# Optimization experiments

Measured on AMD Instinct MI355X. Metric: run time of the kernel, lower is better.

The kernel has to match this reference:

```python
import jax, jax.numpy as jnp
import numpy as np

N = 50000        # nodes
E = 800000       # edges (avg degree 16)
OBS = 128        # observation_dim
HID = 64         # hidden_dim (per head)
H1 = 4           # heads in conv1
ACT = 32         # action_dim
NEG_SLOPE = 0.2  # GATv2 default negative_slope


def setup_inputs() -> dict:
    key = jax.random.key(0)
    ks = jax.random.split(key, 10)
    s = 0.05
    x = jax.random.normal(ks[0], (N, OBS), jnp.float32)
    edge_index = jax.random.randint(ks[1], (2, E), 0, N, dtype=jnp.int32)
    # conv1: GATv2Conv(OBS -> HID, heads=4, concat=True)
    W1l = jax.random.normal(ks[2], (OBS, H1 * HID), jnp.float32) * s  # lin_l (source)
    W1r = jax.random.normal(ks[3], (OBS, H1 * HID), jnp.float32) * s  # lin_r (target)
    att1 = jax.random.normal(ks[4], (H1, HID), jnp.float32) * s
    b1 = jnp.zeros((H1 * HID,), jnp.float32)
    # conv2: GATv2Conv(H1*HID -> ACT, heads=1, concat=False)
    W2l = jax.random.normal(ks[5], (H1 * HID, ACT), jnp.float32) * s
    W2r = jax.random.normal(ks[6], (H1 * HID, ACT), jnp.float32) * s
    att2 = jax.random.normal(ks[7], (1, ACT), jnp.float32) * s
    b2 = jnp.zeros((ACT,), jnp.float32)
    return {"x": x, "edge_index": edge_index, "W1l": W1l, "W1r": W1r,
            "att1": att1, "b1": b1, "W2l": W2l, "W2r": W2r,
            "att2": att2, "b2": b2}


def gatv2_layer(x, Wl, Wr, att, bias, src, dst, heads, out_ch, concat):
    """PyG GATv2Conv (add_self_loops=False, share_weights=False)."""
    n = x.shape[0]
    xl = (x @ Wl).reshape(n, heads, out_ch)  # source transform
    xr = (x @ Wr).reshape(n, heads, out_ch)  # target transform
    e = xl[src] + xr[dst]                    # [E, H, C] gathered messages
    g = jnp.where(e > 0, e, NEG_SLOPE * e)   # LeakyReLU
    logits = jnp.einsum('ehc,hc->eh', g, att)  # [E, H]
    # segment softmax over incoming edges of each destination node
    m = jax.ops.segment_max(logits, dst, num_segments=n)      # [N, H]
    ex = jnp.exp(logits - m[dst])
    denom = jax.ops.segment_sum(ex, dst, num_segments=n)      # [N, H]
    alpha = ex / denom[dst]                                   # [E, H]
    out = jax.ops.segment_sum(xl[src] * alpha[:, :, None], dst, num_segments=n)
    out = out.reshape(n, heads * out_ch) if concat else out.mean(axis=1)
    return out + bias


def reference(x, edge_index, W1l, W1r, att1, b1, W2l, W2r, att2, b2):
    src, dst = edge_index[0], edge_index[1]
    h = jax.nn.relu(gatv2_layer(x, W1l, W1r, att1, b1, src, dst, H1, HID, True))
    out = gatv2_layer(h, W2l, W2r, att2, b2, src, dst, 1, ACT, False)
    return out
```

## Files before the change

### kernel.cpp

```cpp
#include <hip/hip_runtime.h>
#include <hip/hip_bf16.h>
#include <math.h>


#define OBS 128
#define HID 64
#define H1 4
#define C1 256
#define ACT 32
#define PAD 64
#define NEG_SLOPE 0.2f
#define LOG2E 1.4426950408889634f
#define SB 512
#define CAP 8192
#define AGGB 2048

typedef __attribute__((ext_vector_type(2))) _Float16 h2;
typedef __attribute__((ext_vector_type(8))) _Float16 half8;
typedef __attribute__((ext_vector_type(4))) float f32x4;

__device__ inline h2 bc_h2(unsigned u) { return __builtin_bit_cast(h2, u); }
__device__ inline unsigned bc_u(h2 v) { return __builtin_bit_cast(unsigned, v); }
__device__ inline h2 lrelu2(h2 e) {
  const h2 k = {(_Float16)NEG_SLOPE, (_Float16)NEG_SLOPE};
  return __builtin_elementwise_max(e, e * k);
}

__global__ void prep0(const float* __restrict__ W1l, const float* __restrict__ W1r,
                      const float* __restrict__ W2l, const float* __restrict__ W2r,
                      _Float16* __restrict__ W1t, _Float16* __restrict__ W2t,
                      unsigned* __restrict__ bucketCursor) {
  int i = blockIdx.x * 256 + threadIdx.x;
  if (i < 256) bucketCursor[i] = 0;
  if (i < 512 * 128) {
    int n = i >> 7, k = i & 127;
    float v = (n < C1) ? W1l[k * C1 + n] : W1r[k * C1 + (n - C1)];
    W1t[i] = (_Float16)v;
  }
  int j = i - 512 * 128;
  if (j >= 0 && j < 64 * 256) {
    int n = j >> 8, c = j & 255;
    float v = (n < ACT) ? W2l[c * ACT + n] : W2r[c * ACT + (n - ACT)];
    W2t[j] = (_Float16)v;
  }
}

__global__ __launch_bounds__(256) void scat2_k(const int* __restrict__ src,
                                               const int* __restrict__ dst,
                                               unsigned* __restrict__ bucketCursor,
                                               unsigned* __restrict__ sorted,
                                               int E, int epb) {
  __shared__ unsigned cnt[256];
  __shared__ unsigned lbase[256];
  __shared__ unsigned lrank[256];
  int t = threadIdx.x;
  cnt[t] = 0;
  lrank[t] = 0;
  __syncthreads();
  int beg = blockIdx.x * epb;
  int end = beg + epb;
  if (end > E) end = E;
  for (int e = beg + t; e < end; e += 256)
    atomicAdd(&cnt[dst[e] >> 8], 1u);
  __syncthreads();
  unsigned c = cnt[t];
  lbase[t] = c ? atomicAdd(&bucketCursor[t], c) : 0u;
  __syncthreads();
  for (int e = beg + t; e < end; e += 256) {
    int d = dst[e];
    int sv = src[e];
    int b = d >> 8;
    unsigned r = atomicAdd(&lrank[b], 1u);
    sorted[(size_t)b * CAP + lbase[b] + r] =
        ((unsigned)(d & 255) << 16) | (unsigned)sv;
  }
}

__global__ __launch_bounds__(256) void bcsr_k(const unsigned* __restrict__ sorted,
                                              const unsigned* __restrict__ bucketCursor,
                                              unsigned short* __restrict__ esrc_p,
                                              int* __restrict__ cursor, int N) {
  __shared__ unsigned cnt2[256];
  int b = blockIdx.x;
  int t = threadIdx.x;
  cnt2[t] = 0;
  __syncthreads();
  unsigned total = bucketCursor[b];
  const unsigned* sp = sorted + (size_t)b * CAP;
  for (unsigned e = t; e < total; e += 256) {
    unsigned u = sp[e];
    unsigned dl = u >> 16;
    unsigned slot = atomicAdd(&cnt2[dl], 1u);
    if (slot < PAD)
      esrc_p[((size_t)((b << 8) + (int)dl) << 6) + slot] =
          (unsigned short)(u & 0xFFFFu);
  }
  __syncthreads();
  int node = (b << 8) + t;
  if (node < N) cursor[node] = (int)cnt2[t];
}

__global__ __launch_bounds__(256) void gemm1(
    const float* __restrict__ xf,
    const _Float16* __restrict__ W1t,
    _Float16* __restrict__ XLh,
    _Float16* __restrict__ XRh,
    int M) {
  const int LDK = 136;
  __shared__ _Float16 As[128 * 136];
  __shared__ _Float16 Bs[128 * 136];

  const int tid = threadIdx.x;
  const int lane = tid & 63;
  const int wid = tid >> 6;
  const int wm = (wid & 1) * 64, wn = (wid >> 1) * 64;
  const int rowBase = blockIdx.x * 128;
  const int l15 = lane & 15, lq = lane >> 4;

#pragma unroll
  for (int cc = 0; cc < 8; ++cc) {
    int q = cc * 256 + tid;
    int r = q >> 4;
    int kc = (q & 15) * 8;
    int grow = rowBase + r;
    float4 f0 = make_float4(0.f, 0.f, 0.f, 0.f), f1 = f0;
    if (grow < M) {
      f0 = *(const float4*)(xf + (size_t)grow * 128 + kc);
      f1 = *(const float4*)(xf + (size_t)grow * 128 + kc + 4);
    }
    h2 p0 = {(_Float16)f0.x, (_Float16)f0.y};
    h2 p1 = {(_Float16)f0.z, (_Float16)f0.w};
    h2 p2 = {(_Float16)f1.x, (_Float16)f1.y};
    h2 p3 = {(_Float16)f1.z, (_Float16)f1.w};
    *(int4*)(As + r * LDK + kc) = make_int4(bc_u(p0), bc_u(p1), bc_u(p2), bc_u(p3));
  }
#pragma unroll
  for (int cc = 0; cc < 8; ++cc) {
    int q = cc * 256 + tid;
    int r = q >> 4;
    int kc = (q & 15) * 8;
    *(int4*)(Bs + r * LDK + kc) = *(const int4*)(W1t + (size_t)r * 128 + kc);
  }
  __syncthreads();

  for (int cb = 0; cb < 4; ++cb) {
    f32x4 acc[4][4];
#pragma unroll
    for (int i = 0; i < 4; ++i)
#pragma unroll
      for (int j = 0; j < 4; ++j) acc[i][j] = (f32x4){0.f, 0.f, 0.f, 0.f};

#pragma unroll
    for (int ks = 0; ks < 4; ++ks) {
      half8 af[4], bf[4];
#pragma unroll
      for (int t = 0; t < 4; ++t) {
        af[t] = *(const half8*)(As + (wm + t * 16 + l15) * LDK + ks * 32 + lq * 8);
        bf[t] = *(const half8*)(Bs + (wn + t * 16 + l15) * LDK + ks * 32 + lq * 8);
      }
#pragma unroll
      for (int mt = 0; mt < 4; ++mt)
#pragma unroll
        for (int nt = 0; nt < 4; ++nt)
          acc[mt][nt] = __builtin_amdgcn_mfma_f32_16x16x32_f16(
              af[mt], bf[nt], acc[mt][nt], 0, 0, 0);
    }

    _Float16* outp = (cb < 2) ? XLh : XRh;
    int colBase = (cb & 1) * 128;
#pragma unroll
    for (int mt = 0; mt < 4; ++mt) {
#pragma unroll
      for (int r = 0; r < 4; ++r) {
        int row = rowBase + wm + mt * 16 + lq * 4 + r;
        if (row >= M) continue;
#pragma unroll
        for (int nt = 0; nt < 4; ++nt) {
          int col = colBase + wn + nt * 16 + l15;
          outp[(size_t)row * C1 + col] = (_Float16)acc[mt][nt][r];
        }
      }
    }

    if (cb < 3) {
      __syncthreads();
#pragma unroll
      for (int cc = 0; cc < 8; ++cc) {
        int q = cc * 256 + tid;
        int r = q >> 4;
        int kc = (q & 15) * 8;
        *(int4*)(Bs + r * LDK + kc) =
            *(const int4*)(W1t + (size_t)((cb + 1) * 128 + r) * 128 + kc);
      }
      __syncthreads();
    }
  }
}

__global__ __launch_bounds__(256) void gemm_mfma2(
    const _Float16* __restrict__ Hh,
    const _Float16* __restrict__ W2t,
    _Float16* __restrict__ H2h,
    int M) {
  const int LDK = 136;
  __shared__ _Float16 As[128 * 136];
  __shared__ _Float16 Bs[64 * 136];
  const int tid = threadIdx.x;
  const int lane = tid & 63;
  const int wid = tid >> 6;
  const int wm = (wid & 1) * 64, wn = (wid >> 1) * 32;
  const int rowBase = blockIdx.x * 128;

  f32x4 acc[4][2];
#pragma unroll
  for (int i = 0; i < 4; ++i)
#pragma unroll
    for (int j = 0; j < 2; ++j) acc[i][j] = (f32x4){0.f, 0.f, 0.f, 0.f};

  const int l15 = lane & 15, lq = lane >> 4;

  for (int kb = 0; kb < 256; kb += 128) {
#pragma unroll
    for (int cc = 0; cc < 8; ++cc) {
      int q = cc * 256 + tid;
      int r = q >> 4;
      int kc = (q & 15) * 8;
      int grow = rowBase + r;
      int4 av = make_int4(0, 0, 0, 0);
      if (grow < M) av = *(const int4*)(Hh + (size_t)grow * 256 + kb + kc);
      *(int4*)(As + r * LDK + kc) = av;
    }
#pragma unroll
    for (int cc = 0; cc < 4; ++cc) {
      int q = cc * 256 + tid;
      int r = q >> 4;
      int kc = (q & 15) * 8;
      *(int4*)(Bs + r * LDK + kc) = *(const int4*)(W2t + (size_t)r * 256 + kb + kc);
    }
    __syncthreads();

#pragma unroll
    for (int ks = 0; ks < 4; ++ks) {
      half8 af[4], bf[2];
#pragma unroll
      for (int t = 0; t < 4; ++t)
        af[t] = *(const half8*)(As + (wm + t * 16 + l15) * LDK + ks * 32 + lq * 8);
#pragma unroll
      for (int t = 0; t < 2; ++t)
        bf[t] = *(const half8*)(Bs + (wn + t * 16 + l15) * LDK + ks * 32 + lq * 8);
#pragma unroll
      for (int mt = 0; mt < 4; ++mt)
#pragma unroll
        for (int nt = 0; nt < 2; ++nt)
          acc[mt][nt] = __builtin_amdgcn_mfma_f32_16x16x32_f16(
              af[mt], bf[nt], acc[mt][nt], 0, 0, 0);
    }
    __syncthreads();
  }

#pragma unroll
  for (int mt = 0; mt < 4; ++mt) {
#pragma unroll
    for (int r = 0; r < 4; ++r) {
      int row = rowBase + wm + mt * 16 + lq * 4 + r;
      if (row >= M) continue;
#pragma unroll
      for (int nt = 0; nt < 2; ++nt) {
        int col = wn + nt * 16 + l15;
        H2h[(size_t)row * 64 + col] = (_Float16)acc[mt][nt][r];
      }
    }
  }
}

__global__ __launch_bounds__(256) void agg1(const _Float16* __restrict__ XLh,
                                            const _Float16* XRh,
                                            const float* __restrict__ att1,
                                            const float* __restrict__ b1,
                                            const int* __restrict__ degp,
                                            const unsigned short* __restrict__ esrc_p,
                                            _Float16* Hh, int n_nodes) {
  int wave = threadIdx.x >> 6;
  int lane = threadIdx.x & 63;
  int n = blockIdx.x * 4 + wave;
  if (n >= n_nodes) return;
  int sl = lane & 31;
  int half = lane >> 5;
  int c8 = sl * 8;

  const char* XLb = (const char*)XLh + c8 * 2;
  int4 xru = *(const int4*)((const char*)XRh + ((size_t)n << 9) + c8 * 2);
  h2 xr[4] = {bc_h2(xru.x), bc_h2(xru.y), bc_h2(xru.z), bc_h2(xru.w)};
  const float* ap = att1 + (c8 >> 6) * HID + (c8 & 63);
  float4 a0 = *(const float4*)ap;
  float4 a1 = *(const float4*)(ap + 4);
  h2 av[4] = {{(_Float16)(a0.x * LOG2E), (_Float16)(a0.y * LOG2E)},
              {(_Float16)(a0.z * LOG2E), (_Float16)(a0.w * LOG2E)},
              {(_Float16)(a1.x * LOG2E), (_Float16)(a1.y * LOG2E)},
              {(_Float16)(a1.z * LOG2E), (_Float16)(a1.w * LOG2E)}};

  int d = min(degp[n], PAD);
  const unsigned short* ep = esrc_p + ((size_t)n << 6);
  float l = 0.f;
  h2 acc[4];
#pragma unroll
  for (int k = 0; k < 4; ++k) acc[k] = (h2){(_Float16)0.f, (_Float16)0.f};

  int base = 0;
  for (; base + 16 <= d; base += 16) {
    int4 u[8];
#pragma unroll
    for (int t = 0; t < 8; ++t) {
      int s = ep[base + 2 * t + half];
      u[t] = *(const int4*)(XLb + ((size_t)s << 9));
    }
    float c[8];
#pragma unroll
    for (int t = 0; t < 8; ++t) {
      h2 xa = bc_h2(u[t].x), xb = bc_h2(u[t].y), xc = bc_h2(u[t].z), xd = bc_h2(u[t].w);
      float cc = __builtin_amdgcn_fdot2(lrelu2(xa + xr[0]), av[0], 0.f, false);
      cc = __builtin_amdgcn_fdot2(lrelu2(xb + xr[1]), av[1], cc, false);
      cc = __builtin_amdgcn_fdot2(lrelu2(xc + xr[2]), av[2], cc, false);
      cc = __builtin_amdgcn_fdot2(lrelu2(xd + xr[3]), av[3], cc, false);
      c[t] = cc;
    }
#pragma unroll
    for (int t = 0; t < 8; ++t) {
      c[t] += __shfl_xor(c[t], 1);
      c[t] += __shfl_xor(c[t], 2);
      c[t] += __shfl_xor(c[t], 4);
    }
#pragma unroll
    for (int t = 0; t < 8; ++t) {
      float p = __builtin_amdgcn_exp2f(c[t]);
      l += p;
      _Float16 ph = (_Float16)p;
      h2 w = {ph, ph};
      acc[0] = acc[0] + w * bc_h2(u[t].x);
      acc[1] = acc[1] + w * bc_h2(u[t].y);
      acc[2] = acc[2] + w * bc_h2(u[t].z);
      acc[3] = acc[3] + w * bc_h2(u[t].w);
    }
  }
  for (; base + 4 <= d; base += 4) {
    int s0 = ep[base + half];
    int s1 = ep[base + 2 + half];
    int4 u0 = *(const int4*)(XLb + ((size_t)s0 << 9));
    int4 u1 = *(const int4*)(XLb + ((size_t)s1 << 9));
    h2 x0[4] = {bc_h2(u0.x), bc_h2(u0.y), bc_h2(u0.z), bc_h2(u0.w)};
    h2 x1[4] = {bc_h2(u1.x), bc_h2(u1.y), bc_h2(u1.z), bc_h2(u1.w)};
    float c0 = 0.f, c1 = 0.f;
#pragma unroll
    for (int k = 0; k < 4; ++k) {
      c0 = __builtin_amdgcn_fdot2(lrelu2(x0[k] + xr[k]), av[k], c0, false);
      c1 = __builtin_amdgcn_fdot2(lrelu2(x1[k] + xr[k]), av[k], c1, false);
    }
    c0 += __shfl_xor(c0, 1); c1 += __shfl_xor(c1, 1);
    c0 += __shfl_xor(c0, 2); c1 += __shfl_xor(c1, 2);
    c0 += __shfl_xor(c0, 4); c1 += __shfl_xor(c1, 4);
    float p0 = __builtin_amdgcn_exp2f(c0);
    float p1 = __builtin_amdgcn_exp2f(c1);
    l += p0 + p1;
    _Float16 q0 = (_Float16)p0, q1 = (_Float16)p1;
    h2 w0 = {q0, q0}, w1 = {q1, q1};
#pragma unroll
    for (int k = 0; k < 4; ++k) acc[k] = acc[k] + w0 * x0[k] + w1 * x1[k];
  }
  if (base < d) {
    int e0 = base + half, e1 = base + 2 + half;
    bool v0 = e0 < d, v1 = e1 < d;
    int s0 = ep[v0 ? e0 : 0];
    int s1 = ep[v1 ? e1 : 0];
    int4 u0 = *(const int4*)(XLb + ((size_t)s0 << 9));
    int4 u1 = *(const int4*)(XLb + ((size_t)s1 << 9));
    h2 x0[4] = {bc_h2(u0.x), bc_h2(u0.y), bc_h2(u0.z), bc_h2(u0.w)};
    h2 x1[4] = {bc_h2(u1.x), bc_h2(u1.y), bc_h2(u1.z), bc_h2(u1.w)};
    float c0 = 0.f, c1 = 0.f;
#pragma unroll
    for (int k = 0; k < 4; ++k) {
      c0 = __builtin_amdgcn_fdot2(lrelu2(x0[k] + xr[k]), av[k], c0, false);
      c1 = __builtin_amdgcn_fdot2(lrelu2(x1[k] + xr[k]), av[k], c1, false);
    }
    c0 += __shfl_xor(c0, 1); c1 += __shfl_xor(c1, 1);
    c0 += __shfl_xor(c0, 2); c1 += __shfl_xor(c1, 2);
    c0 += __shfl_xor(c0, 4); c1 += __shfl_xor(c1, 4);
    float p0 = v0 ? __builtin_amdgcn_exp2f(c0) : 0.f;
    float p1 = v1 ? __builtin_amdgcn_exp2f(c1) : 0.f;
    l += p0 + p1;
    _Float16 q0 = (_Float16)p0, q1 = (_Float16)p1;
    h2 w0 = {q0, q0}, w1 = {q1, q1};
#pragma unroll
    for (int k = 0; k < 4; ++k) acc[k] = acc[k] + w0 * x0[k] + w1 * x1[k];
  }

  l += __shfl_xor(l, 32);
#pragma unroll
  for (int k = 0; k < 4; ++k) {
    unsigned o = __shfl_xor((int)bc_u(acc[k]), 32);
    acc[k] = acc[k] + bc_h2(o);
  }

  float inv = (d > 0) ? 1.f / l : 0.f;
  if (half == 0) {
    float4 b0 = *(const float4*)(b1 + c8);
    float4 b3 = *(const float4*)(b1 + c8 + 4);
    float o0 = fmaxf((float)acc[0][0] * inv + b0.x, 0.f);
    float o1 = fmaxf((float)acc[0][1] * inv + b0.y, 0.f);
    float o2 = fmaxf((float)acc[1][0] * inv + b0.z, 0.f);
    float o3 = fmaxf((float)acc[1][1] * inv + b0.w, 0.f);
    float o4 = fmaxf((float)acc[2][0] * inv + b3.x, 0.f);
    float o5 = fmaxf((float)acc[2][1] * inv + b3.y, 0.f);
    float o6 = fmaxf((float)acc[3][0] * inv + b3.z, 0.f);
    float o7 = fmaxf((float)acc[3][1] * inv + b3.w, 0.f);
    h2 q0 = {(_Float16)o0, (_Float16)o1};
    h2 q1 = {(_Float16)o2, (_Float16)o3};
    h2 q2 = {(_Float16)o4, (_Float16)o5};
    h2 q3 = {(_Float16)o6, (_Float16)o7};
    *(int4*)((char*)Hh + ((size_t)n << 9) + c8 * 2) =
        make_int4(bc_u(q0), bc_u(q1), bc_u(q2), bc_u(q3));
  }
}

__global__ __launch_bounds__(256) void agg2(const _Float16* __restrict__ H2h,
                                            const float* __restrict__ att2,
                                            const float* __restrict__ b2,
                                            const int* __restrict__ degp,
                                            const unsigned short* __restrict__ esrc_p,
                                            float* __restrict__ out, int n_nodes) {
  int wave = threadIdx.x >> 6;
  int lane = threadIdx.x & 63;
  int wgid = blockIdx.x * 4 + wave;
  int W = gridDim.x * 4;
  int g = lane >> 3;
  int j = lane & 7;
  int c4 = j * 4;

  const char* Hb = (const char*)H2h + c4 * 2;
  float4 af = *(const float4*)(att2 + c4);
  h2 a0 = {(_Float16)(af.x * LOG2E), (_Float16)(af.y * LOG2E)};
  h2 a1 = {(_Float16)(af.z * LOG2E), (_Float16)(af.w * LOG2E)};
  float4 bb = *(const float4*)(b2 + c4);

  for (int n0 = wgid * 2; n0 < n_nodes; n0 += W * 2) {
    int n1 = n0 + 1;
    bool has1 = n1 < n_nodes;
    int n1s = has1 ? n1 : n0;

    uint2 hru0 = *(const uint2*)((const char*)H2h + ((size_t)n0 << 7) + 64 + c4 * 2);
    uint2 hru1 = *(const uint2*)((const char*)H2h + ((size_t)n1s << 7) + 64 + c4 * 2);
    h2 hr00 = bc_h2(hru0.x), hr01 = bc_h2(hru0.y);
    h2 hr10 = bc_h2(hru1.x), hr11 = bc_h2(hru1.y);

    int d0 = min(degp[n0], PAD);
    int d1 = has1 ? min(degp[n1], PAD) : 0;
    const unsigned short* ep0 = esrc_p + ((size_t)n0 << 6);
    const unsigned short* ep1 = esrc_p + ((size_t)n1s << 6);

    float l0 = 0.f, l1 = 0.f;
    h2 z = {(_Float16)0.f, (_Float16)0.f};
    h2 acc00 = z, acc01 = z, acc10 = z, acc11 = z;

    int dmax = d0 > d1 ? d0 : d1;
    for (int base = 0; base < dmax; base += 16) {
      int eA = base + g, eB = base + 8 + g;
      bool vA0 = eA < d0, vB0 = eB < d0;
      bool vA1 = eA < d1, vB1 = eB < d1;
      int sA0 = ep0[vA0 ? eA : 0];
      int sB0 = ep0[vB0 ? eB : 0];
      int sA1 = ep1[vA1 ? eA : 0];
      int sB1 = ep1[vB1 ? eB : 0];
      uint2 uA0 = *(const uint2*)(Hb + ((size_t)sA0 << 7));
      uint2 uB0 = *(const uint2*)(Hb + ((size_t)sB0 << 7));
      uint2 uA1 = *(const uint2*)(Hb + ((size_t)sA1 << 7));
      uint2 uB1 = *(const uint2*)(Hb + ((size_t)sB1 << 7));
      h2 hA0x = bc_h2(uA0.x), hA0y = bc_h2(uA0.y);
      h2 hB0x = bc_h2(uB0.x), hB0y = bc_h2(uB0.y);
      h2 hA1x = bc_h2(uA1.x), hA1y = bc_h2(uA1.y);
      h2 hB1x = bc_h2(uB1.x), hB1y = bc_h2(uB1.y);
      float cA0 = __builtin_amdgcn_fdot2(lrelu2(hA0x + hr00), a0,
                  __builtin_amdgcn_fdot2(lrelu2(hA0y + hr01), a1, 0.f, false), false);
      float cB0 = __builtin_amdgcn_fdot2(lrelu2(hB0x + hr00), a0,
                  __builtin_amdgcn_fdot2(lrelu2(hB0y + hr01), a1, 0.f, false), false);
      float cA1 = __builtin_amdgcn_fdot2(lrelu2(hA1x + hr10), a0,
                  __builtin_amdgcn_fdot2(lrelu2(hA1y + hr11), a1, 0.f, false), false);
      float cB1 = __builtin_amdgcn_fdot2(lrelu2(hB1x + hr10), a0,
                  __builtin_amdgcn_fdot2(lrelu2(hB1y + hr11), a1, 0.f, false), false);
#pragma unroll
      for (int o = 1; o < 8; o <<= 1) {
        cA0 += __shfl_xor(cA0, o); cB0 += __shfl_xor(cB0, o);
        cA1 += __shfl_xor(cA1, o); cB1 += __shfl_xor(cB1, o);
      }
      float pA0 = vA0 ? __builtin_amdgcn_exp2f(cA0) : 0.f;
      float pB0 = vB0 ? __builtin_amdgcn_exp2f(cB0) : 0.f;
      float pA1 = vA1 ? __builtin_amdgcn_exp2f(cA1) : 0.f;
      float pB1 = vB1 ? __builtin_amdgcn_exp2f(cB1) : 0.f;
      l0 += pA0 + pB0;
      l1 += pA1 + pB1;
      _Float16 qA0 = (_Float16)pA0, qB0 = (_Float16)pB0;
      _Float16 qA1 = (_Float16)pA1, qB1 = (_Float16)pB1;
      h2 wA0 = {qA0, qA0}, wB0 = {qB0, qB0};
      h2 wA1 = {qA1, qA1}, wB1 = {qB1, qB1};
      acc00 = acc00 + wA0 * hA0x + wB0 * hB0x;
      acc01 = acc01 + wA0 * hA0y + wB0 * hB0y;
      acc10 = acc10 + wA1 * hA1x + wB1 * hB1x;
      acc11 = acc11 + wA1 * hA1y + wB1 * hB1y;
    }

#pragma unroll
    for (int o = 8; o < 64; o <<= 1) {
      l0 += __shfl_xor(l0, o);
      l1 += __shfl_xor(l1, o);
      acc00 = acc00 + bc_h2((unsigned)__shfl_xor((int)bc_u(acc00), o));
      acc01 = acc01 + bc_h2((unsigned)__shfl_xor((int)bc_u(acc01), o));
      acc10 = acc10 + bc_h2((unsigned)__shfl_xor((int)bc_u(acc10), o));
      acc11 = acc11 + bc_h2((unsigned)__shfl_xor((int)bc_u(acc11), o));
    }

    if (g == 0) {
      float4 o;
      if (d0 > 0) {
        float inv = 1.f / l0;
        o.x = (float)acc00[0] * inv + bb.x;
        o.y = (float)acc00[1] * inv + bb.y;
        o.z = (float)acc01[0] * inv + bb.z;
        o.w = (float)acc01[1] * inv + bb.w;
      } else {
        o = bb;
      }
      *(float4*)(out + (size_t)n0 * ACT + c4) = o;
    } else if (g == 1 && has1) {
      float4 o;
      if (d1 > 0) {
        float inv = 1.f / l1;
        o.x = (float)acc10[0] * inv + bb.x;
        o.y = (float)acc10[1] * inv + bb.y;
        o.z = (float)acc11[0] * inv + bb.z;
        o.w = (float)acc11[1] * inv + bb.w;
      } else {
        o = bb;
      }
      *(float4*)(out + (size_t)n1 * ACT + c4) = o;
    }
  }
}

extern "C" void kernel_launch(void* const* d_in, const int* in_sizes, int n_in,
                              void* d_out, int out_size, void* d_ws, size_t ws_size,
                              hipStream_t stream) {
  (void)n_in; (void)out_size; (void)ws_size;
  const float* x    = (const float*)d_in[0];
  const int*   ei   = (const int*)d_in[1];
  const float* W1l  = (const float*)d_in[2];
  const float* W1r  = (const float*)d_in[3];
  const float* att1 = (const float*)d_in[4];
  const float* b1   = (const float*)d_in[5];
  const float* W2l  = (const float*)d_in[6];
  const float* W2r  = (const float*)d_in[7];
  const float* att2 = (const float*)d_in[8];
  const float* b2   = (const float*)d_in[9];
  float* out = (float*)d_out;

  const int N = in_sizes[0] / OBS;
  const int E = in_sizes[1] / 2;
  const int* src = ei;
  const int* dst = ei + E;

  _Float16* XLh = (_Float16*)d_ws;
  _Float16* XRh = XLh + (size_t)N * C1;
  _Float16* W1t = XRh + (size_t)N * C1;
  _Float16* W2t = W1t + 512 * 128;
  int* cursor   = (int*)(W2t + 64 * 256);
  unsigned short* esrc_p = (unsigned short*)(cursor + N);
  _Float16* Hh  = XRh;
  _Float16* H2h = XLh;

  unsigned* sortedW = (unsigned*)d_ws;
  unsigned* bcur    = sortedW + 256 * CAP;

  dim3 b256(256);
  int gemmBlocks = (N + 127) / 128;
  int prepBlocks = (512 * 128 + 64 * 256 + 255) / 256;
  int NB = (N + 255) >> 8;
  int epb = (E + SB - 1) / SB;
  int aggBlocks = AGGB;
  if (aggBlocks * 8 > N) aggBlocks = (N + 7) / 8;

  prep0<<<prepBlocks, b256, 0, stream>>>(W1l, W1r, W2l, W2r, W1t, W2t, bcur);
  scat2_k<<<SB, b256, 0, stream>>>(src, dst, bcur, sortedW, E, epb);
  bcsr_k<<<NB, b256, 0, stream>>>(sortedW, bcur, esrc_p, cursor, N);
  gemm1<<<gemmBlocks, b256, 0, stream>>>(x, W1t, XLh, XRh, N);
  agg1<<<(N + 3) / 4, b256, 0, stream>>>(XLh, XRh, att1, b1, cursor, esrc_p, Hh, N);
  gemm_mfma2<<<gemmBlocks, b256, 0, stream>>>(Hh, W2t, H2h, N);
  agg2<<<aggBlocks, b256, 0, stream>>>(H2h, att2, b2, cursor, esrc_p, out, N);
}
```

Before: 222.0 us.

## Fuse edge bucket scatter into first GEMM kernel and relocate sort buffer

The edge bucket scatter pass now runs at the start of the first-layer GEMM kernel, so a separate launch disappears and the scatter's atomics and stores can overlap with GEMM work from other blocks. The sorted buffer is moved past esrc_p so it no longer aliases XLh/XRh, which the fused kernel writes at the same time. CAP is reduced and writes past CAP are clamped, so a bucket with more than 6144 edges would silently drop edges. The fused kernel also uses more shared memory and registers, which may lower occupancy for the GEMM part.

```diff
diff --git a/kernel.cpp b/kernel.cpp
--- a/kernel.cpp
+++ b/kernel.cpp
@@ -11,8 +11,7 @@
 #define PAD 64
 #define NEG_SLOPE 0.2f
 #define LOG2E 1.4426950408889634f
-#define SB 512
-#define CAP 8192
+#define CAP 6144
 #define AGGB 2048
 
 typedef __attribute__((ext_vector_type(2))) _Float16 h2;
@@ -45,34 +44,134 @@
   }
 }
 
-__global__ __launch_bounds__(256) void scat2_k(const int* __restrict__ src,
-                                               const int* __restrict__ dst,
-                                               unsigned* __restrict__ bucketCursor,
-                                               unsigned* __restrict__ sorted,
-                                               int E, int epb) {
+__global__ __launch_bounds__(256) void gemm1_sc(
+    const float* __restrict__ xf,
+    const _Float16* __restrict__ W1t,
+    _Float16* __restrict__ XLh,
+    _Float16* __restrict__ XRh,
+    int M,
+    const int* __restrict__ src, const int* __restrict__ dst,
+    unsigned* __restrict__ bcur, unsigned* __restrict__ sorted,
+    int E, int ept) {
+  const int LDK = 136;
+  __shared__ _Float16 As[128 * 136];
+  __shared__ _Float16 Bs[128 * 136];
   __shared__ unsigned cnt[256];
   __shared__ unsigned lbase[256];
   __shared__ unsigned lrank[256];
-  int t = threadIdx.x;
-  cnt[t] = 0;
-  lrank[t] = 0;
+
+  const int tid = threadIdx.x;
+
+  cnt[tid] = 0;
+  lrank[tid] = 0;
   __syncthreads();
-  int beg = blockIdx.x * epb;
-  int end = beg + epb;
-  if (end > E) end = E;
-  for (int e = beg + t; e < end; e += 256)
-    atomicAdd(&cnt[dst[e] >> 8], 1u);
+  int ebase = blockIdx.x * ept * 256;
+  for (int r = 0; r < ept; ++r) {
+    int e = ebase + r * 256 + tid;
+    if (e < E) atomicAdd(&cnt[dst[e] >> 8], 1u);
+  }
   __syncthreads();
-  unsigned c = cnt[t];
-  lbase[t] = c ? atomicAdd(&bucketCursor[t], c) : 0u;
+  {
+    unsigned c = cnt[tid];
+    lbase[tid] = c ? atomicAdd(&bcur[tid], c) : 0u;
+  }
   __syncthreads();
-  for (int e = beg + t; e < end; e += 256) {
-    int d = dst[e];
-    int sv = src[e];
-    int b = d >> 8;
-    unsigned r = atomicAdd(&lrank[b], 1u);
-    sorted[(size_t)b * CAP + lbase[b] + r] =
-        ((unsigned)(d & 255) << 16) | (unsigned)sv;
+  for (int r = 0; r < ept; ++r) {
+    int e = ebase + r * 256 + tid;
+    if (e < E) {
+      int d = dst[e];
+      int b = d >> 8;
+      unsigned rk = atomicAdd(&lrank[b], 1u);
+      unsigned off = lbase[b] + rk;
+      if (off < CAP)
+        sorted[(size_t)b * CAP + off] =
+            ((unsigned)(d & 255) << 16) | (unsigned)src[e];
+    }
+  }
+
+  const int lane = tid & 63;
+  const int wid = tid >> 6;
+  const int wm = (wid & 1) * 64, wn = (wid >> 1) * 64;
+  const int rowBase = blockIdx.x * 128;
+  const int l15 = lane & 15, lq = lane >> 4;
+
+#pragma unroll
+  for (int cc = 0; cc < 8; ++cc) {
+    int q = cc * 256 + tid;
+    int r = q >> 4;
+    int kc = (q & 15) * 8;
+    int grow = rowBase + r;
+    float4 f0 = make_float4(0.f, 0.f, 0.f, 0.f), f1 = f0;
+    if (grow < M) {
+      f0 = *(const float4*)(xf + (size_t)grow * 128 + kc);
+      f1 = *(const float4*)(xf + (size_t)grow * 128 + kc + 4);
+    }
+    h2 p0 = {(_Float16)f0.x, (_Float16)f0.y};
+    h2 p1 = {(_Float16)f0.z, (_Float16)f0.w};
+    h2 p2 = {(_Float16)f1.x, (_Float16)f1.y};
+    h2 p3 = {(_Float16)f1.z, (_Float16)f1.w};
+    *(int4*)(As + r * LDK + kc) = make_int4(bc_u(p0), bc_u(p1), bc_u(p2), bc_u(p3));
+  }
+#pragma unroll
+  for (int cc = 0; cc < 8; ++cc) {
+    int q = cc * 256 + tid;
+    int r = q >> 4;
+    int kc = (q & 15) * 8;
+    *(int4*)(Bs + r * LDK + kc) = *(const int4*)(W1t + (size_t)r * 128 + kc);
+  }
+  __syncthreads();
+
+  for (int cb = 0; cb < 4; ++cb) {
+    f32x4 acc[4][4];
+#pragma unroll
+    for (int i = 0; i < 4; ++i)
+#pragma unroll
+      for (int j = 0; j < 4; ++j) acc[i][j] = (f32x4){0.f, 0.f, 0.f, 0.f};
+
+#pragma unroll
+    for (int ks = 0; ks < 4; ++ks) {
+      half8 af[4], bf[4];
+#pragma unroll
+      for (int t = 0; t < 4; ++t) {
+        af[t] = *(const half8*)(As + (wm + t * 16 + l15) * LDK + ks * 32 + lq * 8);
+        bf[t] = *(const half8*)(Bs + (wn + t * 16 + l15) * LDK + ks * 32 + lq * 8);
+      }
+#pragma unroll
+      for (int mt = 0; mt < 4; ++mt)
+#pragma unroll
+        for (int nt = 0; nt < 4; ++nt)
+          acc[mt][nt] = __builtin_amdgcn_mfma_f32_16x16x32_f16(
+              af[mt], bf[nt], acc[mt][nt], 0, 0, 0);
+    }
+
+    _Float16* outp = (cb < 2) ? XLh : XRh;
+    int colBase = (cb & 1) * 128;
+#pragma unroll
+    for (int mt = 0; mt < 4; ++mt) {
+#pragma unroll
+      for (int r = 0; r < 4; ++r) {
+        int row = rowBase + wm + mt * 16 + lq * 4 + r;
+        if (row >= M) continue;
+#pragma unroll
+        for (int nt = 0; nt < 4; ++nt) {
+          int col = colBase + wn + nt * 16 + l15;
+          outp[(size_t)row * C1 + col] = (_Float16)acc[mt][nt][r];
+        }
+      }
+    }
+
+    if (cb < 3) {
+      __syncthreads();
+#pragma unroll
+      for (int cc = 0; cc < 8; ++cc) {
+        int q = cc * 256 + tid;
+        int r = q >> 4;
+        int kc = (q & 15) * 8;
+        *(int4*)(Bs + r * LDK + kc) =
+            *(const int4*)(W1t + (size_t)((cb + 1) * 128 + r) * 128 + kc);
+      }
+      __syncthreads();
+    }
   }
 }
 
@@ -86,6 +185,7 @@
   cnt2[t] = 0;
   __syncthreads();
   unsigned total = bucketCursor[b];
+  if (total > CAP) total = CAP;
   const unsigned* sp = sorted + (size_t)b * CAP;
   for (unsigned e = t; e < total; e += 256) {
     unsigned u = sp[e];
@@ -98,179 +198,6 @@
   __syncthreads();
   int node = (b << 8) + t;
   if (node < N) cursor[node] = (int)cnt2[t];
-}
-
-__global__ __launch_bounds__(256) void gemm1(
-    const float* __restrict__ xf,
-    const _Float16* __restrict__ W1t,
-    _Float16* __restrict__ XLh,
-    _Float16* __restrict__ XRh,
-    int M) {
-  const int LDK = 136;
-  __shared__ _Float16 As[128 * 136];
-  __shared__ _Float16 Bs[128 * 136];
-
-  const int tid = threadIdx.x;
-  const int lane = tid & 63;
-  const int wid = tid >> 6;
-  const int wm = (wid & 1) * 64, wn = (wid >> 1) * 64;
-  const int rowBase = blockIdx.x * 128;
-  const int l15 = lane & 15, lq = lane >> 4;
-
-#pragma unroll
-  for (int cc = 0; cc < 8; ++cc) {
-    int q = cc * 256 + tid;
-    int r = q >> 4;
-    int kc = (q & 15) * 8;
-    int grow = rowBase + r;
-    float4 f0 = make_float4(0.f, 0.f, 0.f, 0.f), f1 = f0;
-    if (grow < M) {
-      f0 = *(const float4*)(xf + (size_t)grow * 128 + kc);
-      f1 = *(const float4*)(xf + (size_t)grow * 128 + kc + 4);
-    }
-    h2 p0 = {(_Float16)f0.x, (_Float16)f0.y};
-    h2 p1 = {(_Float16)f0.z, (_Float16)f0.w};
-    h2 p2 = {(_Float16)f1.x, (_Float16)f1.y};
-    h2 p3 = {(_Float16)f1.z, (_Float16)f1.w};
-    *(int4*)(As + r * LDK + kc) = make_int4(bc_u(p0), bc_u(p1), bc_u(p2), bc_u(p3));
-  }
-#pragma unroll
-  for (int cc = 0; cc < 8; ++cc) {
-    int q = cc * 256 + tid;
-    int r = q >> 4;
-    int kc = (q & 15) * 8;
-    *(int4*)(Bs + r * LDK + kc) = *(const int4*)(W1t + (size_t)r * 128 + kc);
-  }
-  __syncthreads();
-
-  for (int cb = 0; cb < 4; ++cb) {
-    f32x4 acc[4][4];
-#pragma unroll
-    for (int i = 0; i < 4; ++i)
-#pragma unroll
-      for (int j = 0; j < 4; ++j) acc[i][j] = (f32x4){0.f, 0.f, 0.f, 0.f};
-
-#pragma unroll
-    for (int ks = 0; ks < 4; ++ks) {
-      half8 af[4], bf[4];
-#pragma unroll
-      for (int t = 0; t < 4; ++t) {
-        af[t] = *(const half8*)(As + (wm + t * 16 + l15) * LDK + ks * 32 + lq * 8);
-        bf[t] = *(const half8*)(Bs + (wn + t * 16 + l15) * LDK + ks * 32 + lq * 8);
-      }
-#pragma unroll
-      for (int mt = 0; mt < 4; ++mt)
-#pragma unroll
-        for (int nt = 0; nt < 4; ++nt)
-          acc[mt][nt] = __builtin_amdgcn_mfma_f32_16x16x32_f16(
-              af[mt], bf[nt], acc[mt][nt], 0, 0, 0);
-    }
-
-    _Float16* outp = (cb < 2) ? XLh : XRh;
-    int colBase = (cb & 1) * 128;
-#pragma unroll
-    for (int mt = 0; mt < 4; ++mt) {
-#pragma unroll
-      for (int r = 0; r < 4; ++r) {
-        int row = rowBase + wm + mt * 16 + lq * 4 + r;
-        if (row >= M) continue;
-#pragma unroll
-        for (int nt = 0; nt < 4; ++nt) {
-          int col = colBase + wn + nt * 16 + l15;
-          outp[(size_t)row * C1 + col] = (_Float16)acc[mt][nt][r];
-        }
-      }
-    }
-
-    if (cb < 3) {
-      __syncthreads();
-#pragma unroll
-      for (int cc = 0; cc < 8; ++cc) {
-        int q = cc * 256 + tid;
-        int r = q >> 4;
-        int kc = (q & 15) * 8;
-        *(int4*)(Bs + r * LDK + kc) =
-            *(const int4*)(W1t + (size_t)((cb + 1) * 128 + r) * 128 + kc);
-      }
-      __syncthreads();
-    }
-  }
-}
-
-__global__ __launch_bounds__(256) void gemm_mfma2(
-    const _Float16* __restrict__ Hh,
-    const _Float16* __restrict__ W2t,
-    _Float16* __restrict__ H2h,
-    int M) {
-  const int LDK = 136;
-  __shared__ _Float16 As[128 * 136];
-  __shared__ _Float16 Bs[64 * 136];
-  const int tid = threadIdx.x;
-  const int lane = tid & 63;
-  const int wid = tid >> 6;
-  const int wm = (wid & 1) * 64, wn = (wid >> 1) * 32;
-  const int rowBase = blockIdx.x * 128;
-
-  f32x4 acc[4][2];
-#pragma unroll
-  for (int i = 0; i < 4; ++i)
-#pragma unroll
-    for (int j = 0; j < 2; ++j) acc[i][j] = (f32x4){0.f, 0.f, 0.f, 0.f};
-
-  const int l15 = lane & 15, lq = lane >> 4;
-
-  for (int kb = 0; kb < 256; kb += 128) {
-#pragma unroll
-    for (int cc = 0; cc < 8; ++cc) {
-      int q = cc * 256 + tid;
-      int r = q >> 4;
-      int kc = (q & 15) * 8;
-      int grow = rowBase + r;
-      int4 av = make_int4(0, 0, 0, 0);
-      if (grow < M) av = *(const int4*)(Hh + (size_t)grow * 256 + kb + kc);
-      *(int4*)(As + r * LDK + kc) = av;
-    }
-#pragma unroll
-    for (int cc = 0; cc < 4; ++cc) {
-      int q = cc * 256 + tid;
-      int r = q >> 4;
-      int kc = (q & 15) * 8;
-      *(int4*)(Bs + r * LDK + kc) = *(const int4*)(W2t + (size_t)r * 256 + kb + kc);
-    }
-    __syncthreads();
-
-#pragma unroll
-    for (int ks = 0; ks < 4; ++ks) {
-      half8 af[4], bf[2];
-#pragma unroll
-      for (int t = 0; t < 4; ++t)
-        af[t] = *(const half8*)(As + (wm + t * 16 + l15) * LDK + ks * 32 + lq * 8);
-#pragma unroll
-      for (int t = 0; t < 2; ++t)
-        bf[t] = *(const half8*)(Bs + (wn + t * 16 + l15) * LDK + ks * 32 + lq * 8);
-#pragma unroll
-      for (int mt = 0; mt < 4; ++mt)
-#pragma unroll
-        for (int nt = 0; nt < 2; ++nt)
-          acc[mt][nt] = __builtin_amdgcn_mfma_f32_16x16x32_f16(
-              af[mt], bf[nt], acc[mt][nt], 0, 0, 0);
-    }
-    __syncthreads();
-  }
-
-#pragma unroll
-  for (int mt = 0; mt < 4; ++mt) {
-#pragma unroll
-    for (int r = 0; r < 4; ++r) {
-      int row = rowBase + wm + mt * 16 + lq * 4 + r;
-      if (row >= M) continue;
-#pragma unroll
-      for (int nt = 0; nt < 2; ++nt) {
-        int col = wn + nt * 16 + l15;
-        H2h[(size_t)row * 64 + col] = (_Float16)acc[mt][nt][r];
-      }
-    }
-  }
 }
 
 __global__ __launch_bounds__(256) void agg1(const _Float16* __restrict__ XLh,
@@ -418,6 +345,82 @@
     h2 q3 = {(_Float16)o6, (_Float16)o7};
     *(int4*)((char*)Hh + ((size_t)n << 9) + c8 * 2) =
         make_int4(bc_u(q0), bc_u(q1), bc_u(q2), bc_u(q3));
+  }
+}
+
+__global__ __launch_bounds__(256) void gemm_mfma2(
+    const _Float16* __restrict__ Hh,
+    const _Float16* __restrict__ W2t,
+    _Float16* __restrict__ H2h,
+    int M) {
+  const int LDK = 136;
+  __shared__ _Float16 As[128 * 136];
+  __shared__ _Float16 Bs[64 * 136];
+  const int tid = threadIdx.x;
+  const int lane = tid & 63;
+  const int wid = tid >> 6;
+  const int wm = (wid & 1) * 64, wn = (wid >> 1) * 32;
+  const int rowBase = blockIdx.x * 128;
+
+  f32x4 acc[4][2];
+#pragma unroll
+  for (int i = 0; i < 4; ++i)
+#pragma unroll
+    for (int j = 0; j < 2; ++j) acc[i][j] = (f32x4){0.f, 0.f, 0.f, 0.f};
+
+  const int l15 = lane & 15, lq = lane >> 4;
+
+  for (int kb = 0; kb < 256; kb += 128) {
+#pragma unroll
+    for (int cc = 0; cc < 8; ++cc) {
+      int q = cc * 256 + tid;
+      int r = q >> 4;
+      int kc = (q & 15) * 8;
+      int grow = rowBase + r;
+      int4 av = make_int4(0, 0, 0, 0);
+      if (grow < M) av = *(const int4*)(Hh + (size_t)grow * 256 + kb + kc);
+      *(int4*)(As + r * LDK + kc) = av;
+    }
+#pragma unroll
+    for (int cc = 0; cc < 4; ++cc) {
+      int q = cc * 256 + tid;
+      int r = q >> 4;
+      int kc = (q & 15) * 8;
+      *(int4*)(Bs + r * LDK + kc) = *(const int4*)(W2t + (size_t)r * 256 + kb + kc);
+    }
+    __syncthreads();
+
+#pragma unroll
+    for (int ks = 0; ks < 4; ++ks) {
+      half8 af[4], bf[2];
+#pragma unroll
+      for (int t = 0; t < 4; ++t)
+        af[t] = *(const half8*)(As + (wm + t * 16 + l15) * LDK + ks * 32 + lq * 8);
+#pragma unroll
+      for (int t = 0; t < 2; ++t)
+        bf[t] = *(const half8*)(Bs + (wn + t * 16 + l15) * LDK + ks * 32 + lq * 8);
+#pragma unroll
+      for (int mt = 0; mt < 4; ++mt)
+#pragma unroll
+        for (int nt = 0; nt < 2; ++nt)
+          acc[mt][nt] = __builtin_amdgcn_mfma_f32_16x16x32_f16(
+              af[mt], bf[nt], acc[mt][nt], 0, 0, 0);
+    }
+    __syncthreads();
+  }
+
+#pragma unroll
+  for (int mt = 0; mt < 4; ++mt) {
+#pragma unroll
+    for (int r = 0; r < 4; ++r) {
+      int row = rowBase + wm + mt * 16 + lq * 4 + r;
+      if (row >= M) continue;
+#pragma unroll
+      for (int nt = 0; nt < 2; ++nt) {
+        int col = wn + nt * 16 + l15;
+        H2h[(size_t)row * 64 + col] = (_Float16)acc[mt][nt][r];
+      }
+    }
   }
 }
 
@@ -574,21 +577,21 @@
   _Float16* Hh  = XRh;
   _Float16* H2h = XLh;
 
-  unsigned* sortedW = (unsigned*)d_ws;
-  unsigned* bcur    = sortedW + 256 * CAP;
+  int NB = (N + 255) >> 8;
+  unsigned* sortedW = (unsigned*)(esrc_p + (size_t)N * PAD);
+  unsigned* bcur    = sortedW + (size_t)NB * CAP;
 
   dim3 b256(256);
   int gemmBlocks = (N + 127) / 128;
   int prepBlocks = (512 * 128 + 64 * 256 + 255) / 256;
-  int NB = (N + 255) >> 8;
-  int epb = (E + SB - 1) / SB;
+  int ept = (E + gemmBlocks * 256 - 1) / (gemmBlocks * 256);
   int aggBlocks = AGGB;
   if (aggBlocks * 8 > N) aggBlocks = (N + 7) / 8;
 
   prep0<<<prepBlocks, b256, 0, stream>>>(W1l, W1r, W2l, W2r, W1t, W2t, bcur);
-  scat2_k<<<SB, b256, 0, stream>>>(src, dst, bcur, sortedW, E, epb);
+  gemm1_sc<<<gemmBlocks, b256, 0, stream>>>(
+      x, W1t, XLh, XRh, N, src, dst, bcur, sortedW, E, ept);
   bcsr_k<<<NB, b256, 0, stream>>>(sortedW, bcur, esrc_p, cursor, N);
-  gemm1<<<gemmBlocks, b256, 0, stream>>>(x, W1t, XLh, XRh, N);
   agg1<<<(N + 3) / 4, b256, 0, stream>>>(XLh, XRh, att1, b1, cursor, esrc_p, Hh, N);
   gemm_mfma2<<<gemmBlocks, b256, 0, stream>>>(Hh, W2t, H2h, N);
   agg2<<<aggBlocks, b256, 0, stream>>>(H2h, att2, b2, cursor, esrc_p, out, N);
```

New measurement: 221.0 us (median of 2 runs). Within noise of the previous version (-0.4%).
